# Performance work log

Hardware: AMD Instinct MI355X
Metric: run time of the kernel (lower is better)

The kernel has to match this reference:

```python
import jax, jax.numpy as jnp
import numpy as np

N, C, H, W = 16, 128, 48, 48
CI = C // 2  # inter_channels


def setup_inputs() -> dict:
    key = jax.random.key(0)
    ks = jax.random.split(key, 9)
    s_in = 1.0 / np.sqrt(C)
    s_out = 1.0 / np.sqrt(CI)
    return {
        "features": jax.random.normal(ks[0], (N, C, H, W), jnp.float32),
        "Wq": jax.random.normal(ks[1], (CI, C), jnp.float32) * s_in,
        "bq": jax.random.normal(ks[2], (CI,), jnp.float32) * 0.01,
        "Wk": jax.random.normal(ks[3], (CI, C), jnp.float32) * s_in,
        "bk": jax.random.normal(ks[4], (CI,), jnp.float32) * 0.01,
        "Wv": jax.random.normal(ks[5], (CI, C), jnp.float32) * s_in,
        "bv": jax.random.normal(ks[6], (CI,), jnp.float32) * 0.01,
        "Wz": jax.random.normal(ks[7], (C, CI), jnp.float32) * s_out,
        "bz": jax.random.normal(ks[8], (C,), jnp.float32) * 0.01,
    }


def reference(features, Wq, bq, Wk, bk, Wv, bv, Wz, bz):
    n, c, h, w = features.shape
    hw = h * w

    def proj(x, Wp, bp):
        # conv1x1 over (n, c, h, w) -> tokens (n, hw, ci)
        t = jnp.einsum('nchw,dc->ndhw', x, Wp) + bp[None, :, None, None]
        return t.reshape(n, -1, hw).transpose(0, 2, 1)

    q = proj(features, Wq, bq)   # (n, hw, ci)
    k = proj(features, Wk, bk)
    v = proj(features, Wv, bv)

    # before/after neighbor slices with edge clamping (slice 0 / slice n-1 use themselves)
    kb = jnp.concatenate([k[:1], k[:-1]], axis=0)
    vb = jnp.concatenate([v[:1], v[:-1]], axis=0)
    ka = jnp.concatenate([k[1:], k[-1:]], axis=0)
    va = jnp.concatenate([v[1:], v[-1:]], axis=0)

    def attend(kk, vv):
        f = jnp.einsum('nqd,nkd->nqk', q, kk)        # (n, hw, hw); no 1/sqrt(d) scale, per original
        a = jax.nn.softmax(f, axis=-1)
        y = jnp.einsum('nqk,nkd->nqd', a, vv)        # (n, hw, ci)
        z = jnp.einsum('nqd,cd->nqc', y, Wz) + bz    # W_z conv1x1
        return z.transpose(0, 2, 1).reshape(n, c, h, w)

    return attend(kb, vb) + attend(ka, va) + features
```

## Files before the change

### kernel.cpp

```cpp
#include <hip/hip_runtime.h>
#include <math.h>

#define NBATCH 16
#define CCH    128
#define HW     2304
#define DI     64
#define NTILE  36
#define HTILE  18
#define QBLK   18
#define LOG2E  1.44269504088896f

typedef unsigned short u16;
typedef unsigned int   u32;
typedef __bf16   bf16x8 __attribute__((ext_vector_type(8)));
typedef _Float16 f16x8  __attribute__((ext_vector_type(8)));
typedef float    f32x4  __attribute__((ext_vector_type(4)));

__device__ __forceinline__ u16 f2bf_rne(float x) {
    union { float f; u32 u; } v; v.f = x;
    u32 r = (v.u + 0x7FFFu + ((v.u >> 16) & 1u)) >> 16;
    return (u16)r;
}
__device__ __forceinline__ u16 f2h(float x) {
    union { _Float16 h; u16 u; } c; c.h = (_Float16)x; return c.u;
}
__device__ __forceinline__ float exp2v(float x) {
    float r;
    asm("v_exp_f32 %0, %1" : "=v"(r) : "v"(x));
    return r;
}

__global__ __launch_bounds__(256) void wprep_kernel(
    const float* __restrict__ Wq, const float* __restrict__ Wk,
    const float* __restrict__ Wv, const float* __restrict__ Wz,
    u16* __restrict__ Wf, u16* __restrict__ Wzf)
{
    const int idx  = blockIdx.x * 256 + threadIdx.x;
    if (idx < 3072) {
        const int lane = idx & 63;
        const int fi   = idx >> 6;
        const int g = fi >> 2, ks = fi & 3;
        const int lo = lane & 15, hi = lane >> 4;
        const int row = g * 16 + lo;
        const float* src = (row < 64)  ? &Wq[row * CCH]
                         : (row < 128) ? &Wk[(row - 64) * CCH]
                                       : &Wv[(row - 128) * CCH];
        const int c0 = (ks * 4 + hi) * 8;
        float4 a = *(const float4*)&src[c0];
        float4 b = *(const float4*)&src[c0 + 4];
        union { u16 s8[8]; uint4 v; } pk;
        pk.s8[0] = f2h(a.x); pk.s8[1] = f2h(a.y); pk.s8[2] = f2h(a.z); pk.s8[3] = f2h(a.w);
        pk.s8[4] = f2h(b.x); pk.s8[5] = f2h(b.y); pk.s8[6] = f2h(b.z); pk.s8[7] = f2h(b.w);
        *(uint4*)&Wf[(size_t)idx * 8] = pk.v;
    } else {
        const int t    = idx - 3072;
        const int lane = t & 63;
        const int fi   = t >> 6;
        const int g = fi >> 1, ks = fi & 1;
        const int lo = lane & 15, hi = lane >> 4;
        const int row = g * 16 + lo;
        const int d0  = ks * 32 + hi * 8;
        float4 a = *(const float4*)&Wz[row * DI + d0];
        float4 b = *(const float4*)&Wz[row * DI + d0 + 4];
        union { u16 s8[8]; uint4 v; } pk;
        pk.s8[0] = f2h(a.x); pk.s8[1] = f2h(a.y); pk.s8[2] = f2h(a.z); pk.s8[3] = f2h(a.w);
        pk.s8[4] = f2h(b.x); pk.s8[5] = f2h(b.y); pk.s8[6] = f2h(b.z); pk.s8[7] = f2h(b.w);
        *(uint4*)&Wzf[(size_t)t * 8] = pk.v;
    }
}

__global__ __launch_bounds__(256) void proj_kernel(
    const float* __restrict__ F, const u16* __restrict__ Wf,
    const float* __restrict__ bq, const float* __restrict__ bk,
    const float* __restrict__ bv,
    u16* __restrict__ qo, u16* __restrict__ ko, u16* __restrict__ vto)
{
    __shared__ __align__(16) u16 Fl[64 * 128];
    __shared__ __align__(16) u16 Vt[64 * 72];

    const int tid  = threadIdx.x;
    const int n    = blockIdx.x / NTILE;
    const int p0   = (blockIdx.x % NTILE) * 64;
    const int lane = tid & 63, wave = tid >> 6;
    const int lo   = lane & 15, hi = lane >> 4;

    const float* Fn = F + (size_t)n * CCH * HW;
    #pragma unroll
    for (int i = 0; i < 4; ++i) {
        int s  = tid + i * 256;
        int c0 = (s >> 4) * 2;
        int t0 = (s & 15) * 4;
        const float* fp_ = &Fn[(size_t)c0 * HW + p0 + t0];
        float4 fa = *(const float4*)fp_;
        float4 fb = *(const float4*)(fp_ + HW);
        #pragma unroll
        for (int e = 0; e < 4; ++e) {
            int t = t0 + e;
            u32 w = (u32)f2h((&fa.x)[e]) | ((u32)f2h((&fb.x)[e]) << 16);
            *(u32*)&Fl[t * 128 + (((c0 >> 3) ^ (t & 15)) << 3) + (c0 & 7)] = w;
        }
    }
    __syncthreads();

    const int arow = wave * 16 + lo;
    f16x8 af[4];
    #pragma unroll
    for (int ks = 0; ks < 4; ++ks)
        af[ks] = *(const f16x8*)&Fl[arow * 128 + (((ks * 4 + hi) ^ lo) << 3)];

    f32x4 acc[12];
    #pragma unroll
    for (int g = 0; g < 12; ++g)
        #pragma unroll
        for (int r = 0; r < 4; ++r) acc[g][r] = 0.f;

    #pragma unroll
    for (int g = 0; g < 12; ++g) {
        #pragma unroll
        for (int ks = 0; ks < 4; ++ks) {
            f16x8 bf = *(const f16x8*)&Wf[(size_t)((g * 4 + ks) * 64 + lane) * 8];
            acc[g] = __builtin_amdgcn_mfma_f32_16x16x32_f16(af[ks], bf, acc[g], 0, 0, 0);
        }
    }

    const int twb = p0 + wave * 16 + 4 * hi;
    #pragma unroll
    for (int g = 0; g < 4; ++g) {
        float bQ = bq[g * 16 + lo], bK = bk[g * 16 + lo];
        #pragma unroll
        for (int r = 0; r < 4; ++r) {
            size_t off = ((size_t)n * HW + twb + r) * DI + g * 16 + lo;
            qo[off] = f2h((acc[g][r] + bQ) * LOG2E);
            ko[off] = f2h(acc[g + 4][r] + bK);
        }
    }
    #pragma unroll
    for (int g = 0; g < 4; ++g) {
        float bV = bv[g * 16 + lo];
        #pragma unroll
        for (int r = 0; r < 4; ++r)
            Vt[(g * 16 + lo) * 72 + wave * 16 + 4 * hi + r] = f2bf_rne(acc[g + 8][r] + bV);
    }
    __syncthreads();
    #pragma unroll
    for (int i = 0; i < 2; ++i) {
        int s = tid + i * 256;
        int d = s >> 3, c8 = (s & 7) * 8;
        *(uint4*)&vto[((size_t)n * DI + d) * HW + p0 + c8] = *(const uint4*)&Vt[d * 72 + c8];
    }
}

__global__ __launch_bounds__(256) void attn_pass_kernel(
    const u16* __restrict__ q, const u16* __restrict__ k, const u16* __restrict__ vt,
    float* __restrict__ outF, float* __restrict__ lp)
{
    __shared__ __align__(16) u16 smem[16384];
    u16* const Kb0 = smem;
    u16* const Kb1 = smem + 4096;
    u16* const Vb0 = smem + 8192;
    u16* const Vb1 = smem + 12288;

    const int tid  = threadIdx.x;
    const int lane = tid & 63;
    const int w4   = tid >> 6;
    const int lo   = lane & 15, hi = lane >> 4;

    const int bid  = (int)blockIdx.x;
    const int w    = (bid & 7) * 144 + (bid >> 3);
    const int j    = w / (NBATCH * QBLK);
    const int rem  = w % (NBATCH * QBLK);
    const int n    = rem / QBLK;
    const int qb   = rem % QBLK;
    const int pass = j >> 1, half = j & 1;
    const int P0   = qb * 128;

    const int nb = (pass == 0) ? (n > 0 ? n - 1 : 0)
                               : (n < NBATCH - 1 ? n + 1 : n);
    const u16* kp = k  + (size_t)nb * HW * DI;
    const u16* vp = vt + (size_t)nb * DI * HW;
    const int  kq = half * (HTILE * 64);

    f16x8 qfA0, qfA1, qfB0, qfB1;
    {
        const u16* qp = q + ((size_t)n * HW + P0 + w4 * 32 + lo) * DI + hi * 8;
        qfA0 = *(const f16x8*)qp;
        qfA1 = *(const f16x8*)(qp + 32);
        qfB0 = *(const f16x8*)(qp + 16 * DI);
        qfB1 = *(const f16x8*)(qp + 16 * DI + 32);
    }

    bf16x8 vone;
    #pragma unroll
    for (int e = 0; e < 8; ++e) vone[e] = (__bf16)1.0f;

    const int sch   = tid & 7;
    const int srow0 = tid >> 3;
    const int srow1 = srow0 + 32;
    const int fk0   = (srow0 & 3) | ((srow0 & 8) >> 1);
    const int fk1   = (srow1 & 3) | ((srow1 & 8) >> 1);
    const int koff0 = srow0 * 64 + ((sch ^ fk0) * 8);
    const int koff1 = srow1 * 64 + ((sch ^ fk1) * 8);
    const int voff0 = srow0 * 64 + ((sch ^ (srow0 & 7)) * 8);
    const int voff1 = srow1 * 64 + ((sch ^ (srow1 & 7)) * 8);

    const int krbase = 8 * (lo >> 2) + (lo & 3);
    const int xl = lo & 7;

    f32x4 yaccA[4], yaccB[4], laccA4, laccB4;
    #pragma unroll
    for (int nf = 0; nf < 4; ++nf)
        #pragma unroll
        for (int r = 0; r < 4; ++r) { yaccA[nf][r] = 0.f; yaccB[nf][r] = 0.f; }
    #pragma unroll
    for (int r = 0; r < 4; ++r) { laccA4[r] = 0.f; laccB4[r] = 0.f; }

    uint4 ka0 = *(const uint4*)(kp + (size_t)(kq + srow0) * DI + sch * 8);
    uint4 ka1 = *(const uint4*)(kp + (size_t)(kq + srow1) * DI + sch * 8);
    uint4 va0 = *(const uint4*)(vp + (size_t)srow0 * HW + kq + sch * 8);
    uint4 va1 = *(const uint4*)(vp + (size_t)srow1 * HW + kq + sch * 8);
    *(uint4*)&Kb0[koff0] = ka0;  *(uint4*)&Kb0[koff1] = ka1;
    *(uint4*)&Vb0[voff0] = va0;  *(uint4*)&Vb0[voff1] = va1;
    ka0 = *(const uint4*)(kp + (size_t)(kq + 64 + srow0) * DI + sch * 8);
    ka1 = *(const uint4*)(kp + (size_t)(kq + 64 + srow1) * DI + sch * 8);
    va0 = *(const uint4*)(vp + (size_t)srow0 * HW + kq + 64 + sch * 8);
    va1 = *(const uint4*)(vp + (size_t)srow1 * HW + kq + 64 + sch * 8);
    __syncthreads();

    auto body = [&](int t, const u16* Kc, const u16* Vc, u16* Kn, u16* Vn) {
        if (t + 1 < HTILE) {
            *(uint4*)&Kn[koff0] = ka0; *(uint4*)&Kn[koff1] = ka1;
            *(uint4*)&Vn[voff0] = va0; *(uint4*)&Vn[voff1] = va1;
        }
        if (t + 2 < HTILE) {
            int tb = kq + (t + 2) * 64;
            ka0 = *(const uint4*)(kp + (size_t)(tb + srow0) * DI + sch * 8);
            ka1 = *(const uint4*)(kp + (size_t)(tb + srow1) * DI + sch * 8);
            va0 = *(const uint4*)(vp + (size_t)srow0 * HW + tb + sch * 8);
            va1 = *(const uint4*)(vp + (size_t)srow1 * HW + tb + sch * 8);
        }

        f32x4 stA[4], stB[4];
        __builtin_amdgcn_s_setprio(1);
        #pragma unroll
        for (int m = 0; m < 4; ++m) {
            const int kr = krbase + 4 * (m & 1) + 32 * (m >> 1);
            f16x8 a0 = *(const f16x8*)&Kc[kr * 64 + ((hi ^ xl) * 8)];
            f16x8 a1 = *(const f16x8*)&Kc[kr * 64 + (((4 + hi) ^ xl) * 8)];
            f32x4 zA = {0.f, 0.f, 0.f, 0.f};
            zA = __builtin_amdgcn_mfma_f32_16x16x32_f16(a0, qfA0, zA, 0, 0, 0);
            zA = __builtin_amdgcn_mfma_f32_16x16x32_f16(a1, qfA1, zA, 0, 0, 0);
            stA[m] = zA;
            f32x4 zB = {0.f, 0.f, 0.f, 0.f};
            zB = __builtin_amdgcn_mfma_f32_16x16x32_f16(a0, qfB0, zB, 0, 0, 0);
            zB = __builtin_amdgcn_mfma_f32_16x16x32_f16(a1, qfB1, zB, 0, 0, 0);
            stB[m] = zB;
        }
        __builtin_amdgcn_s_setprio(0);

        bf16x8 paA0, paA1, paB0, paB1;
        #pragma unroll
        for (int m = 0; m < 4; ++m) {
            __bf16 b0 = (__bf16)exp2v(stA[m][0]);
            __bf16 b1 = (__bf16)exp2v(stA[m][1]);
            __bf16 b2 = (__bf16)exp2v(stA[m][2]);
            __bf16 b3 = (__bf16)exp2v(stA[m][3]);
            if (m == 0)      { paA0[0] = b0; paA0[1] = b1; paA0[2] = b2; paA0[3] = b3; }
            else if (m == 1) { paA0[4] = b0; paA0[5] = b1; paA0[6] = b2; paA0[7] = b3; }
            else if (m == 2) { paA1[0] = b0; paA1[1] = b1; paA1[2] = b2; paA1[3] = b3; }
            else             { paA1[4] = b0; paA1[5] = b1; paA1[6] = b2; paA1[7] = b3; }
        }
        #pragma unroll
        for (int m = 0; m < 4; ++m) {
            __bf16 b0 = (__bf16)exp2v(stB[m][0]);
            __bf16 b1 = (__bf16)exp2v(stB[m][1]);
            __bf16 b2 = (__bf16)exp2v(stB[m][2]);
            __bf16 b3 = (__bf16)exp2v(stB[m][3]);
            if (m == 0)      { paB0[0] = b0; paB0[1] = b1; paB0[2] = b2; paB0[3] = b3; }
            else if (m == 1) { paB0[4] = b0; paB0[5] = b1; paB0[6] = b2; paB0[7] = b3; }
            else if (m == 2) { paB1[0] = b0; paB1[1] = b1; paB1[2] = b2; paB1[3] = b3; }
            else             { paB1[4] = b0; paB1[5] = b1; paB1[6] = b2; paB1[7] = b3; }
        }

        __builtin_amdgcn_s_setprio(1);
        laccA4 = __builtin_amdgcn_mfma_f32_16x16x32_bf16(paA0, vone, laccA4, 0, 0, 0);
        laccA4 = __builtin_amdgcn_mfma_f32_16x16x32_bf16(paA1, vone, laccA4, 0, 0, 0);
        laccB4 = __builtin_amdgcn_mfma_f32_16x16x32_bf16(paB0, vone, laccB4, 0, 0, 0);
        laccB4 = __builtin_amdgcn_mfma_f32_16x16x32_bf16(paB1, vone, laccB4, 0, 0, 0);
        #pragma unroll
        for (int nf = 0; nf < 4; ++nf) {
            const int vr = nf * 16 + lo;
            bf16x8 v0 = *(const bf16x8*)&Vc[vr * 64 + ((hi ^ xl) * 8)];
            bf16x8 v1 = *(const bf16x8*)&Vc[vr * 64 + (((4 + hi) ^ xl) * 8)];
            yaccA[nf] = __builtin_amdgcn_mfma_f32_16x16x32_bf16(paA0, v0, yaccA[nf], 0, 0, 0);
            yaccA[nf] = __builtin_amdgcn_mfma_f32_16x16x32_bf16(paA1, v1, yaccA[nf], 0, 0, 0);
            yaccB[nf] = __builtin_amdgcn_mfma_f32_16x16x32_bf16(paB0, v0, yaccB[nf], 0, 0, 0);
            yaccB[nf] = __builtin_amdgcn_mfma_f32_16x16x32_bf16(paB1, v1, yaccB[nf], 0, 0, 0);
        }
        __builtin_amdgcn_s_setprio(0);

        __syncthreads();
    };

    #pragma unroll 1
    for (int tt = 0; tt < HTILE; tt += 2) {
        body(tt,     Kb0, Vb0, Kb1, Vb1);
        body(tt + 1, Kb1, Vb1, Kb0, Vb0);
    }

    float invqA[4], invqB[4];
    #pragma unroll
    for (int r = 0; r < 4; ++r) {
        invqA[r] = 1.f / laccA4[r];
        invqB[r] = 1.f / laccB4[r];
    }
    if (lo == 0) {
        size_t lb = ((size_t)j * NBATCH + n) * HW + P0 + w4 * 32;
        #pragma unroll
        for (int r = 0; r < 4; ++r) {
            lp[lb + 4 * hi + r]      = laccA4[r];
            lp[lb + 16 + 4 * hi + r] = laccB4[r];
        }
    }

    __syncthreads();
    u16* yw = smem;
    #pragma unroll
    for (int nf = 0; nf < 4; ++nf)
        #pragma unroll
        for (int r = 0; r < 4; ++r) {
            yw[(w4 * 32 + 4 * hi + r) * 72 + nf * 16 + lo]      = f2h(yaccA[nf][r] * invqA[r]);
            yw[(w4 * 32 + 16 + 4 * hi + r) * 72 + nf * 16 + lo] = f2h(yaccB[nf][r] * invqB[r]);
        }
    __syncthreads();

    u32* outb = (u32*)outF + (size_t)n * CCH * HW + (size_t)j * 32 * HW;
    const int ptb = P0 >> 6;
    #pragma unroll
    for (int s = 0; s < 4; ++s) {
        int idx = tid + s * 256;
        int T   = idx >> 3, d0 = (idx & 7) * 8;
        int tok = T & 63;
        int f   = (tok >> 1) * HW + (ptb + (T >> 6)) * 64 + (tok & 1) * 32 + (d0 >> 1);
        *(uint4*)&outb[f] = *(const uint4*)&yw[T * 72 + d0];
    }
}

__global__ __launch_bounds__(256) void combine_kernel(
    float* __restrict__ outF, const float* __restrict__ lp,
    const u16* __restrict__ Wzf, const float* __restrict__ bz,
    const float* __restrict__ F)
{
    __shared__ __align__(16) float zs[64 * 129];
    const int tid  = threadIdx.x;
    const int n    = blockIdx.x / NTILE;
    const int p0   = (blockIdx.x % NTILE) * 64;
    const int lane = tid & 63, wave = tid >> 6;
    const int lo   = lane & 15, hi = lane >> 4;
    const int tok  = wave * 16 + lo;

    const u32* pb = (const u32*)outF + (size_t)n * CCH * HW;
    f16x8 af[4][2];
    #pragma unroll
    for (int jj = 0; jj < 4; ++jj)
        #pragma unroll
        for (int ks = 0; ks < 2; ++ks)
            af[jj][ks] = *(const f16x8*)&pb[(size_t)(jj * 32 + (tok >> 1)) * HW
                                            + p0 + (tok & 1) * 32 + ks * 16 + hi * 4];
    float lw[4];
    #pragma unroll
    for (int jj = 0; jj < 4; ++jj)
        lw[jj] = lp[((size_t)jj * NBATCH + n) * HW + p0 + tok];
    float s0 = 1.f / (lw[0] + lw[1]);
    float s1 = 1.f / (lw[2] + lw[3]);
    _Float16 w00 = (_Float16)(lw[0] * s0), w01 = (_Float16)(lw[1] * s0);
    _Float16 w10 = (_Float16)(lw[2] * s1), w11 = (_Float16)(lw[3] * s1);
    f16x8 a00 = af[0][0] * w00 + af[1][0] * w01;
    f16x8 a01 = af[0][1] * w00 + af[1][1] * w01;
    f16x8 a10 = af[2][0] * w10 + af[3][0] * w11;
    f16x8 a11 = af[2][1] * w10 + af[3][1] * w11;

    f32x4 acc[8];
    #pragma unroll
    for (int g = 0; g < 8; ++g)
        #pragma unroll
        for (int r = 0; r < 4; ++r) acc[g][r] = 0.f;

    #pragma unroll
    for (int g = 0; g < 8; ++g) {
        f16x8 b0 = *(const f16x8*)&Wzf[(size_t)((g * 2 + 0) * 64 + lane) * 8];
        f16x8 b1 = *(const f16x8*)&Wzf[(size_t)((g * 2 + 1) * 64 + lane) * 8];
        acc[g] = __builtin_amdgcn_mfma_f32_16x16x32_f16(a00, b0, acc[g], 0, 0, 0);
        acc[g] = __builtin_amdgcn_mfma_f32_16x16x32_f16(a01, b1, acc[g], 0, 0, 0);
        acc[g] = __builtin_amdgcn_mfma_f32_16x16x32_f16(a10, b0, acc[g], 0, 0, 0);
        acc[g] = __builtin_amdgcn_mfma_f32_16x16x32_f16(a11, b1, acc[g], 0, 0, 0);
    }

    #pragma unroll
    for (int g = 0; g < 8; ++g)
        #pragma unroll
        for (int r = 0; r < 4; ++r)
            zs[(wave * 16 + 4 * hi + r) * 129 + g * 16 + lo] = acc[g][r];
    __syncthreads();

    #pragma unroll 4
    for (int i = 0; i < 32; ++i) {
        int c = wave + 4 * i;
        size_t gi = (size_t)(n * CCH + c) * HW + p0 + lane;
        outF[gi] = zs[lane * 129 + c] + 2.f * bz[c] + F[gi];
    }
}

extern "C" void kernel_launch(void* const* d_in, const int* in_sizes, int n_in,
                              void* d_out, int out_size, void* d_ws, size_t ws_size,
                              hipStream_t stream) {
    const float* F  = (const float*)d_in[0];
    const float* Wq = (const float*)d_in[1];
    const float* bq = (const float*)d_in[2];
    const float* Wk = (const float*)d_in[3];
    const float* bk = (const float*)d_in[4];
    const float* Wv = (const float*)d_in[5];
    const float* bv = (const float*)d_in[6];
    const float* Wz = (const float*)d_in[7];
    const float* bz = (const float*)d_in[8];
    float* outp = (float*)d_out;

    const size_t tok = (size_t)NBATCH * HW * DI;
    u16*   qb  = (u16*)d_ws;
    u16*   kb  = qb  + tok;
    u16*   vtb = kb  + tok;
    u16*   wf  = vtb + tok;
    u16*   wzf = wf  + 24576;
    float* lpb = (float*)(wzf + 8192);

    wprep_kernel<<<16, 256, 0, stream>>>(Wq, Wk, Wv, Wz, wf, wzf);
    proj_kernel<<<NBATCH * NTILE, 256, 0, stream>>>(F, wf, bq, bk, bv, qb, kb, vtb);
    attn_pass_kernel<<<4 * NBATCH * QBLK, 256, 0, stream>>>(qb, kb, vtb, outp, lpb);
    combine_kernel<<<NBATCH * NTILE, 256, 0, stream>>>(outp, lpb, wzf, bz, F);
}
```

Before: 89.95 us.

## Load K/V tiles directly into LDS via global_load_lds with source-side swizzle

Replaces the register-staged K/V prefetch (global load into VGPRs, then ds_write to the swizzled LDS slot) with direct global-to-LDS loads. The swizzle moves from the LDS destination to the global source address, so each thread writes a contiguous 16-byte LDS slot. Prefetch depth drops from two tiles ahead, held in registers, to one tile ahead in the other LDS buffer. This removes VGPR pressure and the LDS write instructions, but gives up some latency hiding and depends on hardware support for 16-byte direct LDS loads.

After: 90.36 us. About the same (+0.5%).

```diff
diff --git a/kernel.cpp b/kernel.cpp
--- a/kernel.cpp
+++ b/kernel.cpp
@@ -28,6 +28,11 @@
     float r;
     asm("v_exp_f32 %0, %1" : "=v"(r) : "v"(x));
     return r;
+}
+__device__ __forceinline__ void gld16(const u16* g, u16* l) {
+    __builtin_amdgcn_global_load_lds(
+        (const __attribute__((address_space(1))) u32*)(const void*)g,
+        (__attribute__((address_space(3))) u32*)(void*)l, 16, 0, 0);
 }
 
 __global__ __launch_bounds__(256) void wprep_kernel(
@@ -198,10 +203,12 @@
     const int srow1 = srow0 + 32;
     const int fk0   = (srow0 & 3) | ((srow0 & 8) >> 1);
     const int fk1   = (srow1 & 3) | ((srow1 & 8) >> 1);
-    const int koff0 = srow0 * 64 + ((sch ^ fk0) * 8);
-    const int koff1 = srow1 * 64 + ((sch ^ fk1) * 8);
-    const int voff0 = srow0 * 64 + ((sch ^ (srow0 & 7)) * 8);
-    const int voff1 = srow1 * 64 + ((sch ^ (srow1 & 7)) * 8);
+    const int kcs0  = (sch ^ fk0) * 8;
+    const int kcs1  = (sch ^ fk1) * 8;
+    const int vcs0  = (sch ^ (srow0 & 7)) * 8;
+    const int vcs1  = (sch ^ (srow1 & 7)) * 8;
+    const int ld0   = tid * 8;
+    const int ld1   = tid * 8 + 2048;
 
     const int krbase = 8 * (lo >> 2) + (lo & 3);
     const int xl = lo & 7;
@@ -214,29 +221,19 @@
     #pragma unroll
     for (int r = 0; r < 4; ++r) { laccA4[r] = 0.f; laccB4[r] = 0.f; }
 
-    uint4 ka0 = *(const uint4*)(kp + (size_t)(kq + srow0) * DI + sch * 8);
-    uint4 ka1 = *(const uint4*)(kp + (size_t)(kq + srow1) * DI + sch * 8);
-    uint4 va0 = *(const uint4*)(vp + (size_t)srow0 * HW + kq + sch * 8);
-    uint4 va1 = *(const uint4*)(vp + (size_t)srow1 * HW + kq + sch * 8);
-    *(uint4*)&Kb0[koff0] = ka0;  *(uint4*)&Kb0[koff1] = ka1;
-    *(uint4*)&Vb0[voff0] = va0;  *(uint4*)&Vb0[voff1] = va1;
-    ka0 = *(const uint4*)(kp + (size_t)(kq + 64 + srow0) * DI + sch * 8);
-    ka1 = *(const uint4*)(kp + (size_t)(kq + 64 + srow1) * DI + sch * 8);
-    va0 = *(const uint4*)(vp + (size_t)srow0 * HW + kq + 64 + sch * 8);
-    va1 = *(const uint4*)(vp + (size_t)srow1 * HW + kq + 64 + sch * 8);
+    gld16(kp + (size_t)(kq + srow0) * DI + kcs0, &Kb0[ld0]);
+    gld16(kp + (size_t)(kq + srow1) * DI + kcs1, &Kb0[ld1]);
+    gld16(vp + (size_t)srow0 * HW + kq + vcs0,   &Vb0[ld0]);
+    gld16(vp + (size_t)srow1 * HW + kq + vcs1,   &Vb0[ld1]);
     __syncthreads();
 
     auto body = [&](int t, const u16* Kc, const u16* Vc, u16* Kn, u16* Vn) {
         if (t + 1 < HTILE) {
-            *(uint4*)&Kn[koff0] = ka0; *(uint4*)&Kn[koff1] = ka1;
-            *(uint4*)&Vn[voff0] = va0; *(uint4*)&Vn[voff1] = va1;
-        }
-        if (t + 2 < HTILE) {
-            int tb = kq + (t + 2) * 64;
-            ka0 = *(const uint4*)(kp + (size_t)(tb + srow0) * DI + sch * 8);
-            ka1 = *(const uint4*)(kp + (size_t)(tb + srow1) * DI + sch * 8);
-            va0 = *(const uint4*)(vp + (size_t)srow0 * HW + tb + sch * 8);
-            va1 = *(const uint4*)(vp + (size_t)srow1 * HW + tb + sch * 8);
+            int tb = kq + (t + 1) * 64;
+            gld16(kp + (size_t)(tb + srow0) * DI + kcs0, &Kn[ld0]);
+            gld16(kp + (size_t)(tb + srow1) * DI + kcs1, &Kn[ld1]);
+            gld16(vp + (size_t)srow0 * HW + tb + vcs0,   &Vn[ld0]);
+            gld16(vp + (size_t)srow1 * HW + tb + vcs1,   &Vn[ld1]);
         }
 
         f32x4 stA[4], stB[4];
```
